# Kernel optimization log

Measured on AMD Instinct MI355X. Metric: run time of the kernel, lower is better.

## Reference

```python
import jax, jax.numpy as jnp
import numpy as np

PI = float(np.pi)


def setup_inputs() -> dict:
    key = jax.random.key(0)
    k1, k2 = jax.random.split(key)
    src = jax.random.normal(k1, (32, 4, 512, 512), dtype=jnp.float32)
    fc2 = jax.random.normal(k2, (32, 7), dtype=jnp.float32)
    return {"src": src, "fc2": fc2}


def _build_mat(fc2):
    # Parameter extraction exactly as in the torch module.
    theta = jnp.clip(fc2[:, 0] * 0.3, -1.0, 1.0) * PI          # rotation angle
    scale = jnp.clip(fc2[:, 1:3] * 0.3 + 1.0, 0.0, 5.0)
    trans = fc2[:, 3:5] * 0.3
    shear = jnp.clip(fc2[:, 5:7] * 0.3, -1.0, 1.0) * PI
    sx, sy = scale[:, 0], scale[:, 1]
    tx, ty = trans[:, 0], trans[:, 1]
    shxy, shyx = shear[:, 0], shear[:, 1]
    c, s = jnp.cos(theta), jnp.sin(theta)
    z, o = jnp.zeros_like(c), jnp.ones_like(c)

    def m3(rows):  # rows: list of 3 lists of 3 (B,) scalars -> (B,3,3)
        return jnp.stack([jnp.stack(r, axis=-1) for r in rows], axis=-2)

    # Note: the torch code stacks rows at dim=2 (making the transpose) then
    # transposes (1,2) back, so the effective matrices are the ones as-written.
    rot = m3([[c, -s, z], [s, c, z], [z, z, o]])
    scl = m3([[sx, z, z], [z, sy, z], [z, z, o]])
    shr = m3([[o, shxy, z], [shyx, o, z], [z, z, o]])
    trn = m3([[o, z, tx], [z, o, ty], [z, z, o]])
    # mat = T @ Sh @ S @ R  (batched 3x3 matmuls)
    return trn @ shr @ scl @ rot


def _affine_grid(theta2x3, H, W):
    # F.affine_grid with align_corners=False (the torch default used here):
    # pixel centers map to x=(2w+1)/W-1, y=(2h+1)/H-1.
    xs = (2.0 * jnp.arange(W, dtype=jnp.float32) + 1.0) / W - 1.0  # (W,)
    ys = (2.0 * jnp.arange(H, dtype=jnp.float32) + 1.0) / H - 1.0  # (H,)
    base = jnp.stack([
        jnp.broadcast_to(xs[None, :], (H, W)),
        jnp.broadcast_to(ys[:, None], (H, W)),
        jnp.ones((H, W), dtype=jnp.float32),
    ], axis=-1)                                                     # (H,W,3)
    return jnp.einsum('bij,hwj->bhwi', theta2x3, base)              # (B,H,W,2)


def _grid_sample(src, grid):
    # bilinear, padding_mode='zeros', align_corners=False
    B, C, H, W = src.shape
    ix = ((grid[..., 0] + 1.0) * W - 1.0) * 0.5  # (B,H,W) source x coords
    iy = ((grid[..., 1] + 1.0) * H - 1.0) * 0.5
    x0 = jnp.floor(ix)
    y0 = jnp.floor(iy)
    wx = ix - x0  # frac weights
    wy = iy - y0
    x0i = x0.astype(jnp.int32)
    y0i = y0.astype(jnp.int32)

    def gather(img, xi, yi):  # img (C,H,W); xi,yi (H,W) int
        valid = ((xi >= 0) & (xi < W) & (yi >= 0) & (yi < H)).astype(img.dtype)
        v = img[:, jnp.clip(yi, 0, H - 1), jnp.clip(xi, 0, W - 1)]  # (C,H,W)
        return v * valid[None]

    def per_batch(img, x0i, y0i, wx, wy):
        v00 = gather(img, x0i, y0i)
        v01 = gather(img, x0i + 1, y0i)
        v10 = gather(img, x0i, y0i + 1)
        v11 = gather(img, x0i + 1, y0i + 1)
        return (v00 * (1 - wx) * (1 - wy) + v01 * wx * (1 - wy)
                + v10 * (1 - wx) * wy + v11 * wx * wy)

    return jax.vmap(per_batch)(src, x0i, y0i, wx, wy)


def reference(src, fc2):
    H, W = src.shape[2], src.shape[3]
    mat = _build_mat(fc2)                     # (B,3,3)
    inv_mat = jnp.linalg.inv(mat)             # (B,3,3)
    grid = _affine_grid(mat[:, :2, :], H, W)
    inv_grid = _affine_grid(inv_mat[:, :2, :], H, W)
    transformed = _grid_sample(src, grid)
    return transformed, mat, inv_mat, grid, inv_grid
```

## Files before the change

### kernel.cpp

```cpp
#include <hip/hip_runtime.h>
#include <hip/hip_bf16.h>

#define PI_F 3.14159265358979323846f

__global__ void build_mats_kernel(const float* __restrict__ fc2,
                                  float* __restrict__ mat_out,
                                  float* __restrict__ inv_out,
                                  int B) {
    int b = blockIdx.x * blockDim.x + threadIdx.x;
    if (b >= B) return;
    const float* f = fc2 + b * 7;
    float theta = fminf(fmaxf(f[0] * 0.3f, -1.f), 1.f) * PI_F;
    float sx    = fminf(fmaxf(f[1] * 0.3f + 1.f, 0.f), 5.f);
    float sy    = fminf(fmaxf(f[2] * 0.3f + 1.f, 0.f), 5.f);
    float tx    = f[3] * 0.3f;
    float ty    = f[4] * 0.3f;
    float shxy  = fminf(fmaxf(f[5] * 0.3f, -1.f), 1.f) * PI_F;
    float shyx  = fminf(fmaxf(f[6] * 0.3f, -1.f), 1.f) * PI_F;

    float c = cosf(theta), s = sinf(theta);
    float m00 =  sx * c + shxy * sy * s;
    float m01 = -sx * s + shxy * sy * c;
    float m02 = tx;
    float m10 = shyx * sx * c + sy * s;
    float m11 = -shyx * sx * s + sy * c;
    float m12 = ty;

    float* m = mat_out + b * 9;
    m[0] = m00; m[1] = m01; m[2] = m02;
    m[3] = m10; m[4] = m11; m[5] = m12;
    m[6] = 0.f; m[7] = 0.f; m[8] = 1.f;

    float det = m00 * m11 - m01 * m10;
    float id  = 1.f / det;
    float i00 =  m11 * id, i01 = -m01 * id;
    float i10 = -m10 * id, i11 =  m00 * id;
    float i02 = -(i00 * m02 + i01 * m12);
    float i12 = -(i10 * m02 + i11 * m12);

    float* im = inv_out + b * 9;
    im[0] = i00; im[1] = i01; im[2] = i02;
    im[3] = i10; im[4] = i11; im[5] = i12;
    im[6] = 0.f; im[7] = 0.f; im[8] = 1.f;
}

__global__ __launch_bounds__(256) void affine_main_kernel(
    const float* __restrict__ src,
    const float* __restrict__ mat,
    const float* __restrict__ inv_mat,
    float* __restrict__ transformed,
    float* __restrict__ grid_out,
    float* __restrict__ inv_grid_out)
{
    const int W = 512, H = 512, C = 4;
    int w = blockIdx.x * blockDim.x + threadIdx.x;
    int h = blockIdx.y;
    int b = blockIdx.z;

    float xs = (2.f * (float)w + 1.f) * (1.f / (float)W) - 1.f;
    float ys = (2.f * (float)h + 1.f) * (1.f / (float)H) - 1.f;

    const float* m  = mat + b * 9;
    const float* im = inv_mat + b * 9;
    float gx  = m[0] * xs + m[1] * ys + m[2];
    float gy  = m[3] * xs + m[4] * ys + m[5];
    float igx = im[0] * xs + im[1] * ys + im[2];
    float igy = im[3] * xs + im[4] * ys + im[5];

    size_t pix = ((size_t)b * H + h) * W + w;
    ((float2*)grid_out)[pix]     = make_float2(gx, gy);
    ((float2*)inv_grid_out)[pix] = make_float2(igx, igy);

    float ix = ((gx + 1.f) * (float)W - 1.f) * 0.5f;
    float iy = ((gy + 1.f) * (float)H - 1.f) * 0.5f;
    float x0f = floorf(ix), y0f = floorf(iy);
    float wx = ix - x0f, wy = iy - y0f;
    int x0 = (int)x0f, y0 = (int)y0f;
    int x1 = x0 + 1,   y1 = y0 + 1;

    bool vx0 = (x0 >= 0) && (x0 < W);
    bool vx1 = (x1 >= 0) && (x1 < W);
    bool vy0 = (y0 >= 0) && (y0 < H);
    bool vy1 = (y1 >= 0) && (y1 < H);
    int cx0 = min(max(x0, 0), W - 1), cx1 = min(max(x1, 0), W - 1);
    int cy0 = min(max(y0, 0), H - 1), cy1 = min(max(y1, 0), H - 1);

    float w00 = (1.f - wx) * (1.f - wy) * ((vx0 && vy0) ? 1.f : 0.f);
    float w01 = wx * (1.f - wy)         * ((vx1 && vy0) ? 1.f : 0.f);
    float w10 = (1.f - wx) * wy         * ((vx0 && vy1) ? 1.f : 0.f);
    float w11 = wx * wy                 * ((vx1 && vy1) ? 1.f : 0.f);

    const float* sb = src + (size_t)b * C * H * W;
    size_t o00 = (size_t)cy0 * W + cx0;
    size_t o01 = (size_t)cy0 * W + cx1;
    size_t o10 = (size_t)cy1 * W + cx0;
    size_t o11 = (size_t)cy1 * W + cx1;

    #pragma unroll
    for (int c = 0; c < C; ++c) {
        const float* sc = sb + (size_t)c * H * W;
        float v = sc[o00] * w00 + sc[o01] * w01 + sc[o10] * w10 + sc[o11] * w11;
        transformed[(((size_t)b * C + c) * H + h) * W + w] = v;
    }
}

extern "C" void kernel_launch(void* const* d_in, const int* in_sizes, int n_in,
                              void* d_out, int out_size, void* d_ws, size_t ws_size,
                              hipStream_t stream) {
    const float* src = (const float*)d_in[0];
    const float* fc2 = (const float*)d_in[1];

    const int B = 32, C = 4, H = 512, W = 512;
    float* out = (float*)d_out;

    float* transformed  = out;
    float* mat_out      = out + (size_t)B * C * H * W;
    float* inv_out      = mat_out + (size_t)B * 9;
    float* grid_out     = inv_out + (size_t)B * 9;
    float* inv_grid_out = grid_out + (size_t)B * H * W * 2;

    build_mats_kernel<<<1, 64, 0, stream>>>(fc2, mat_out, inv_out, B);

    dim3 grid(W / 256, H, B);
    dim3 block(256);
    affine_main_kernel<<<grid, block, 0, stream>>>(src, mat_out, inv_out,
                                                   transformed, grid_out, inv_grid_out);
}
```

Measured before the change: 477.0 us.

## Process four pixels per thread with vectorized nontemporal stores

Each thread now handles four consecutive output pixels in a row. It hoists the per-row matrix terms and writes the grid, inverse grid and transformed outputs with 128-bit nontemporal stores. The block shape becomes 128x2 covering two full rows, and the gather offsets switch to 32-bit. The aim is fewer store instructions and less cache pollution on the write-heavy outputs. In exchange, each thread has more registers in flight, and neighbouring threads' gathers are now spread further apart, which may hurt load coalescing.

```diff
diff --git a/kernel.cpp b/kernel.cpp
--- a/kernel.cpp
+++ b/kernel.cpp
@@ -2,6 +2,8 @@
 #include <hip/hip_bf16.h>
 
 #define PI_F 3.14159265358979323846f
+
+typedef float fvec4 __attribute__((ext_vector_type(4)));
 
 __global__ void build_mats_kernel(const float* __restrict__ fc2,
                                   float* __restrict__ mat_out,
@@ -53,54 +55,89 @@
     float* __restrict__ inv_grid_out)
 {
     const int W = 512, H = 512, C = 4;
-    int w = blockIdx.x * blockDim.x + threadIdx.x;
-    int h = blockIdx.y;
-    int b = blockIdx.z;
-
-    float xs = (2.f * (float)w + 1.f) * (1.f / (float)W) - 1.f;
-    float ys = (2.f * (float)h + 1.f) * (1.f / (float)H) - 1.f;
+    int w0 = threadIdx.x * 4;
+    int h  = blockIdx.y * 2 + threadIdx.y;
+    int b  = blockIdx.z;
 
     const float* m  = mat + b * 9;
     const float* im = inv_mat + b * 9;
-    float gx  = m[0] * xs + m[1] * ys + m[2];
-    float gy  = m[3] * xs + m[4] * ys + m[5];
-    float igx = im[0] * xs + im[1] * ys + im[2];
-    float igy = im[3] * xs + im[4] * ys + im[5];
+    float m00 = m[0],  m01 = m[1],  m02 = m[2];
+    float m10 = m[3],  m11 = m[4],  m12 = m[5];
+    float i00 = im[0], i01 = im[1], i02 = im[2];
+    float i10 = im[3], i11 = im[4], i12 = im[5];
 
-    size_t pix = ((size_t)b * H + h) * W + w;
-    ((float2*)grid_out)[pix]     = make_float2(gx, gy);
-    ((float2*)inv_grid_out)[pix] = make_float2(igx, igy);
+    float ys = (2.f * (float)h + 1.f) * (1.f / (float)H) - 1.f;
+    float gyc  = m01 * ys + m02;
+    float gyc2 = m11 * ys + m12;
+    float iyc  = i01 * ys + i02;
+    float iyc2 = i11 * ys + i12;
 
-    float ix = ((gx + 1.f) * (float)W - 1.f) * 0.5f;
-    float iy = ((gy + 1.f) * (float)H - 1.f) * 0.5f;
-    float x0f = floorf(ix), y0f = floorf(iy);
-    float wx = ix - x0f, wy = iy - y0f;
-    int x0 = (int)x0f, y0 = (int)y0f;
-    int x1 = x0 + 1,   y1 = y0 + 1;
+    float gx[4], gy[4], igx[4], igy[4];
+    int   off[4][4];
+    float wt[4][4];
 
-    bool vx0 = (x0 >= 0) && (x0 < W);
-    bool vx1 = (x1 >= 0) && (x1 < W);
-    bool vy0 = (y0 >= 0) && (y0 < H);
-    bool vy1 = (y1 >= 0) && (y1 < H);
-    int cx0 = min(max(x0, 0), W - 1), cx1 = min(max(x1, 0), W - 1);
-    int cy0 = min(max(y0, 0), H - 1), cy1 = min(max(y1, 0), H - 1);
+    #pragma unroll
+    for (int p = 0; p < 4; ++p) {
+        float xs = (2.f * (float)(w0 + p) + 1.f) * (1.f / (float)W) - 1.f;
+        gx[p]  = m00 * xs + gyc;
+        gy[p]  = m10 * xs + gyc2;
+        igx[p] = i00 * xs + iyc;
+        igy[p] = i10 * xs + iyc2;
 
-    float w00 = (1.f - wx) * (1.f - wy) * ((vx0 && vy0) ? 1.f : 0.f);
-    float w01 = wx * (1.f - wy)         * ((vx1 && vy0) ? 1.f : 0.f);
-    float w10 = (1.f - wx) * wy         * ((vx0 && vy1) ? 1.f : 0.f);
-    float w11 = wx * wy                 * ((vx1 && vy1) ? 1.f : 0.f);
+        float ix = ((gx[p] + 1.f) * (float)W - 1.f) * 0.5f;
+        float iy = ((gy[p] + 1.f) * (float)H - 1.f) * 0.5f;
+        float x0f = floorf(ix), y0f = floorf(iy);
+        float wx = ix - x0f, wy = iy - y0f;
+        int x0 = (int)x0f, y0 = (int)y0f;
+        int x1 = x0 + 1,   y1 = y0 + 1;
+
+        bool vx0 = (x0 >= 0) && (x0 < W);
+        bool vx1 = (x1 >= 0) && (x1 < W);
+        bool vy0 = (y0 >= 0) && (y0 < H);
+        bool vy1 = (y1 >= 0) && (y1 < H);
+        int cx0 = min(max(x0, 0), W - 1), cx1 = min(max(x1, 0), W - 1);
+        int cy0 = min(max(y0, 0), H - 1), cy1 = min(max(y1, 0), H - 1);
+
+        wt[p][0] = (1.f - wx) * (1.f - wy) * ((vx0 && vy0) ? 1.f : 0.f);
+        wt[p][1] = wx * (1.f - wy)         * ((vx1 && vy0) ? 1.f : 0.f);
+        wt[p][2] = (1.f - wx) * wy         * ((vx0 && vy1) ? 1.f : 0.f);
+        wt[p][3] = wx * wy                 * ((vx1 && vy1) ? 1.f : 0.f);
+
+        off[p][0] = cy0 * W + cx0;
+        off[p][1] = cy0 * W + cx1;
+        off[p][2] = cy1 * W + cx0;
+        off[p][3] = cy1 * W + cx1;
+    }
+
+    size_t pix = ((size_t)b * H + h) * W + w0;
+    fvec4* gq  = (fvec4*)(grid_out     + pix * 2);
+    fvec4* igq = (fvec4*)(inv_grid_out + pix * 2);
+    fvec4 g0  = {gx[0],  gy[0],  gx[1],  gy[1]};
+    fvec4 g1  = {gx[2],  gy[2],  gx[3],  gy[3]};
+    fvec4 ig0 = {igx[0], igy[0], igx[1], igy[1]};
+    fvec4 ig1 = {igx[2], igy[2], igx[3], igy[3]};
+    __builtin_nontemporal_store(g0,  gq);
+    __builtin_nontemporal_store(g1,  gq + 1);
+    __builtin_nontemporal_store(ig0, igq);
+    __builtin_nontemporal_store(ig1, igq + 1);
 
     const float* sb = src + (size_t)b * C * H * W;
-    size_t o00 = (size_t)cy0 * W + cx0;
-    size_t o01 = (size_t)cy0 * W + cx1;
-    size_t o10 = (size_t)cy1 * W + cx0;
-    size_t o11 = (size_t)cy1 * W + cx1;
-
     #pragma unroll
     for (int c = 0; c < C; ++c) {
         const float* sc = sb + (size_t)c * H * W;
-        float v = sc[o00] * w00 + sc[o01] * w01 + sc[o10] * w10 + sc[o11] * w11;
-        transformed[(((size_t)b * C + c) * H + h) * W + w] = v;
+        float r00 = sc[off[0][0]], r01 = sc[off[0][1]], r02 = sc[off[0][2]], r03 = sc[off[0][3]];
+        float r10 = sc[off[1][0]], r11 = sc[off[1][1]], r12 = sc[off[1][2]], r13 = sc[off[1][3]];
+        float r20 = sc[off[2][0]], r21 = sc[off[2][1]], r22 = sc[off[2][2]], r23 = sc[off[2][3]];
+        float r30 = sc[off[3][0]], r31 = sc[off[3][1]], r32 = sc[off[3][2]], r33 = sc[off[3][3]];
+
+        fvec4 v;
+        v.x = r00 * wt[0][0] + r01 * wt[0][1] + r02 * wt[0][2] + r03 * wt[0][3];
+        v.y = r10 * wt[1][0] + r11 * wt[1][1] + r12 * wt[1][2] + r13 * wt[1][3];
+        v.z = r20 * wt[2][0] + r21 * wt[2][1] + r22 * wt[2][2] + r23 * wt[2][3];
+        v.w = r30 * wt[3][0] + r31 * wt[3][1] + r32 * wt[3][2] + r33 * wt[3][3];
+
+        fvec4* dst = (fvec4*)(transformed + (((size_t)b * C + c) * H + h) * W + w0);
+        __builtin_nontemporal_store(v, dst);
     }
 }
 
@@ -121,8 +158,8 @@
 
     build_mats_kernel<<<1, 64, 0, stream>>>(fc2, mat_out, inv_out, B);
 
-    dim3 grid(W / 256, H, B);
-    dim3 block(256);
+    dim3 grid(1, H / 2, B);
+    dim3 block(128, 2);
     affine_main_kernel<<<grid, block, 0, stream>>>(src, mat_out, inv_out,
                                                    transformed, grid_out, inv_grid_out);
 }
```

Result: slower. 504.5 us (+5.8%).
